# Optimization experiments

Hardware: AMD Instinct MI355X
Metric: run time of the kernel (lower is better)

Reference implementation:

```python
import jax, jax.numpy as jnp
import numpy as np
from jax import lax

B, V, H, W = 8, 3, 512, 640


def setup_inputs() -> dict:
    key = jax.random.key(0)
    k1, k2, k3 = jax.random.split(key, 3)
    # predicted depths in a realistic positive range
    pred_pts = jax.random.uniform(k1, (B, V, H, W), jnp.float32, 1.0, 10.0)
    # pinhole intrinsics embedded in 4x4 (invertible)
    f = 500.0
    K1 = jnp.array([[f, 0.0, (W - 1) / 2.0, 0.0],
                    [0.0, f, (H - 1) / 2.0, 0.0],
                    [0.0, 0.0, 1.0, 0.0],
                    [0.0, 0.0, 0.0, 1.0]], jnp.float32)
    K = jnp.broadcast_to(K1, (B, 4, 4))
    # near-identity rotations (QR of I + small noise) + small translations
    A = jnp.eye(3, dtype=jnp.float32) + 0.05 * jax.random.normal(k2, (B, V, 3, 3), jnp.float32)
    Q, R = jnp.linalg.qr(A)
    Q = Q * jnp.sign(jnp.diagonal(R, axis1=-2, axis2=-1))[..., None, :]
    t = 0.1 * jax.random.normal(k3, (B, V, 3), jnp.float32)
    RT = (jnp.zeros((B, V, 4, 4), jnp.float32)
          .at[..., :3, :3].set(Q)
          .at[..., :3, 3].set(t)
          .at[..., 3, 3].set(1.0))
    return {"pred_pts": pred_pts, "K": K, "input_RTs": RT}


def _bilinear_sample(img_flat, gx, gy, h, w):
    """grid_sample(mode=bilinear, align_corners=False, padding=zeros).
    img_flat: (B, H*W); gx, gy: (B, N) in [-1, 1] grid coords."""
    ix = ((gx + 1.0) * w - 1.0) * 0.5
    iy = ((gy + 1.0) * h - 1.0) * 0.5
    x0f = jnp.floor(ix)
    y0f = jnp.floor(iy)
    wx1 = ix - x0f
    wy1 = iy - y0f
    x0 = x0f.astype(jnp.int32)
    y0 = y0f.astype(jnp.int32)

    def corner(xi, yi):
        valid = (xi >= 0) & (xi < w) & (yi >= 0) & (yi < h)
        idx = jnp.clip(yi, 0, h - 1) * w + jnp.clip(xi, 0, w - 1)
        val = jnp.take_along_axis(img_flat, idx, axis=1)
        return jnp.where(valid, val, 0.0)

    return ((1.0 - wy1) * (1.0 - wx1) * corner(x0, y0)
            + (1.0 - wy1) * wx1 * corner(x0 + 1, y0)
            + wy1 * (1.0 - wx1) * corner(x0, y0 + 1)
            + wy1 * wx1 * corner(x0 + 1, y0 + 1))


def reference(pred_pts, K, input_RTs):
    b, v, h, w = pred_pts.shape
    dt = pred_pts.dtype
    yy, xx = jnp.meshgrid(jnp.arange(h, dtype=dt), jnp.arange(w, dtype=dt), indexing='ij')
    x = xx.reshape(-1)  # (HW,)
    y = yy.reshape(-1)
    Kinv = jnp.linalg.inv(K)            # (B,4,4)
    RTinv = jnp.linalg.inv(input_RTs)   # (B,V,4,4)

    total = jnp.zeros((), dt)
    for i in range(v):
        for j in range(v):
            d = pred_pts[:, i].reshape(b, -1)          # (B, HW)
            ones = jnp.ones_like(d)
            # homogeneous coords (x*d, y*d, d, 1): (B, 4, HW)
            xyz = jnp.stack([x[None] * d, y[None] * d, d, ones], axis=1)
            # composed projection: K @ RT_j @ inv(RT_i) @ inv(K)  (same math as chained bmms)
            P = jnp.einsum('bij,bjk,bkl,blm->bim', K, input_RTs[:, j], RTinv[:, i], Kinv)
            proj = jnp.einsum('bij,bjn->bin', P, xyz)  # (B, 4, HW)
            proj = proj / proj[:, 3:4]
            projected_depth = proj[:, 2]               # (B, HW)
            gx = proj[:, 0] / ((w - 1) / 2.0) - 1.0
            gy = proj[:, 1] / ((h - 1) / 2.0) - 1.0
            mask = ((gx >= -1.0) & (gx <= 1.0) & (gy >= -1.0) & (gy <= 1.0)).astype(dt)
            warped = _bilinear_sample(pred_pts[:, j].reshape(b, -1), gx, gy, h, w)
            num = jnp.sum(jnp.abs(warped - projected_depth) * mask)
            den = jnp.maximum(jnp.sum(mask), 1.0)
            total = total + num / den
    return total
```

## Files before the change

### kernel.cpp

```cpp
#include <hip/hip_runtime.h>

#define Bn 8
#define Vn 3
#define Hn 512
#define Wn 640
#define Nn (Hn * Wn)
#define PX 16
#define TPB 256
#define XBLKS (Nn / (TPB * PX))
#define GRIDN (XBLKS * Vn * Bn)

struct __attribute__((aligned(4))) fpair { float a, b; };

__device__ __forceinline__ float rfl(float x) {
    return __int_as_float(__builtin_amdgcn_readfirstlane(__float_as_int(x)));
}

__device__ __forceinline__ void computeQ(const float* __restrict__ K,
                                         const float* __restrict__ RT,
                                         int b, int i, float Q[Vn][12]) {
    const float* Kb = K + (size_t)b * 16;
    const float f  = Kb[0], cx = Kb[2], cy = Kb[6];
    const float rf = 1.0f / f;
    const float* Ti = RT + (size_t)(b * Vn + i) * 16;
    const float A00=Ti[0], A01=Ti[1], A02=Ti[2],  A03=Ti[3];
    const float A10=Ti[4], A11=Ti[5], A12=Ti[6],  A13=Ti[7];
    const float A20=Ti[8], A21=Ti[9], A22=Ti[10], A23=Ti[11];
    const float I00=A00, I01=A10, I02=A20, I03=-(A00*A03 + A10*A13 + A20*A23);
    const float I10=A01, I11=A11, I12=A21, I13=-(A01*A03 + A11*A13 + A21*A23);
    const float I20=A02, I21=A12, I22=A22, I23=-(A02*A03 + A12*A13 + A22*A23);
    #pragma unroll
    for (int j = 0; j < Vn; ++j) {
        const float* Tj = RT + (size_t)(b * Vn + j) * 16;
        const float B00=Tj[0], B01=Tj[1], B02=Tj[2],  B03=Tj[3];
        const float B10=Tj[4], B11=Tj[5], B12=Tj[6],  B13=Tj[7];
        const float B20=Tj[8], B21=Tj[9], B22=Tj[10], B23=Tj[11];
        const float M00=B00*I00+B01*I10+B02*I20, M01=B00*I01+B01*I11+B02*I21,
                    M02=B00*I02+B01*I12+B02*I22, M03=B00*I03+B01*I13+B02*I23+B03;
        const float M10=B10*I00+B11*I10+B12*I20, M11=B10*I01+B11*I11+B12*I21,
                    M12=B10*I02+B11*I12+B12*I22, M13=B10*I03+B11*I13+B12*I23+B13;
        const float M20=B20*I00+B21*I10+B22*I20, M21=B20*I01+B21*I11+B22*I21,
                    M22=B20*I02+B21*I12+B22*I22, M23=B20*I03+B21*I13+B22*I23+B23;
        const float G00=f*M00+cx*M20, G01=f*M01+cx*M21, G02=f*M02+cx*M22, G03=f*M03+cx*M23;
        const float G10=f*M10+cy*M20, G11=f*M11+cy*M21, G12=f*M12+cy*M22, G13=f*M13+cy*M23;
        const float G20=M20,          G21=M21,          G22=M22,          G23=M23;
        Q[j][0]  = rfl(G00*rf);  Q[j][1]  = rfl(G01*rf);
        Q[j][2]  = rfl(G02 - (cx*rf)*G00 - (cy*rf)*G01);  Q[j][3]  = rfl(G03);
        Q[j][4]  = rfl(G10*rf);  Q[j][5]  = rfl(G11*rf);
        Q[j][6]  = rfl(G12 - (cx*rf)*G10 - (cy*rf)*G11);  Q[j][7]  = rfl(G13);
        Q[j][8]  = rfl(G20*rf);  Q[j][9]  = rfl(G21*rf);
        Q[j][10] = rfl(G22 - (cx*rf)*G20 - (cy*rf)*G21);  Q[j][11] = rfl(G23);
    }
}

__global__ __launch_bounds__(TPB, 8) void loss_main_kernel(const float* __restrict__ pred,
                                                           const float* __restrict__ K,
                                                           const float* __restrict__ RT,
                                                           float* __restrict__ part) {
    const int id   = blockIdx.x;
    const int b    = id & 7;
    const int r    = id >> 3;
    const int i    = r % Vn;
    const int xblk = r / Vn;

    float Q[Vn][12];
    computeQ(K, RT, b, i, Q);

    const int tid  = threadIdx.x;
    const int h    = (xblk >= 40) ? 1 : 0;
    const int c0   = xblk - 40 * h;
    const int yrow = 2 * tid + h;
    int c = c0 + tid;
    c -= (c / 40) * 40;
    const int xcol = c << 4;
    const int base = yrow * Wn + xcol;
    const float fy = (float)yrow;

    const float* dptr = pred + (size_t)(b * Vn + i) * Nn + base;
    float dv[PX];
    {
        const float4 a0 = *reinterpret_cast<const float4*>(dptr);
        const float4 a1 = *reinterpret_cast<const float4*>(dptr + 4);
        const float4 a2 = *reinterpret_cast<const float4*>(dptr + 8);
        const float4 a3 = *reinterpret_cast<const float4*>(dptr + 12);
        dv[0]=a0.x; dv[1]=a0.y; dv[2]=a0.z; dv[3]=a0.w;
        dv[4]=a1.x; dv[5]=a1.y; dv[6]=a1.z; dv[7]=a1.w;
        dv[8]=a2.x; dv[9]=a2.y; dv[10]=a2.z; dv[11]=a2.w;
        dv[12]=a3.x; dv[13]=a3.y; dv[14]=a3.z; dv[15]=a3.w;
    }

    const float cW = (float)Wn / (float)(Wn - 1);
    const float cH = (float)Hn / (float)(Hn - 1);

    float num[Vn] = {0.0f, 0.0f, 0.0f};
    float den[Vn] = {0.0f, 0.0f, 0.0f};

    #pragma unroll
    for (int j = 0; j < Vn; ++j) {
        const float* __restrict__ img = pred + (size_t)(b * Vn + j) * Nn;
        const float rx = fmaf(Q[j][1], fy, Q[j][2]);
        const float ry = fmaf(Q[j][5], fy, Q[j][6]);
        const float rz = fmaf(Q[j][9], fy, Q[j][10]);

        #pragma unroll
        for (int k = 0; k < PX; ++k) {
            const float d  = dv[k];
            const float fx = (float)(xcol + k);

            const float X = fmaf(d, fmaf(Q[j][0], fx, rx), Q[j][3]);
            const float Y = fmaf(d, fmaf(Q[j][4], fx, ry), Q[j][7]);
            const float Z = fmaf(d, fmaf(Q[j][8], fx, rz), Q[j][11]);

            const bool inb = (X >= 0.0f) & (X <= (float)(Wn - 1)) &
                             (Y >= 0.0f) & (Y <= (float)(Hn - 1));
            if (inb) {
                const float ix = fmaf(X, cW, -0.5f);
                const float iy = fmaf(Y, cH, -0.5f);
                const float x0f = floorf(ix);
                const float y0f = floorf(iy);
                const float wx1 = ix - x0f;
                const float wy1 = iy - y0f;
                const float wx0 = 1.0f - wx1;
                const float wy0 = 1.0f - wy1;
                const int x0 = (int)x0f;
                const int y0 = (int)y0f;
                const bool border = (x0 < 0) | (x0 > Wn - 2) | (y0 < 0) | (y0 > Hn - 2);
                float warped;
                if (__ballot(border) == 0ull) {
                    const int ad = y0 * Wn + x0;
                    const fpair q0 = *reinterpret_cast<const fpair*>(img + ad);
                    const fpair q1 = *reinterpret_cast<const fpair*>(img + ad + Wn);
                    warped = wy0 * fmaf(wx0, q0.a, wx1 * q0.b)
                           + wy1 * fmaf(wx0, q1.a, wx1 * q1.b);
                } else {
                    const int x1 = x0 + 1;
                    const int y1 = y0 + 1;
                    const int cy0 = max(y0, 0);
                    const int cy1 = min(y1, Hn - 1);
                    const int cx  = min(max(x0, 0), Wn - 2);
                    const bool xlo = (x0 >= 0);
                    const bool xhi = (x0 <= Wn - 2);
                    const fpair q0 = *reinterpret_cast<const fpair*>(img + (cy0 * Wn + cx));
                    const fpair q1 = *reinterpret_cast<const fpair*>(img + (cy1 * Wn + cx));
                    const float c00 = xhi ? q0.a : q0.b;
                    const float c10 = xlo ? q0.b : q0.a;
                    const float c01 = xhi ? q1.a : q1.b;
                    const float c11 = xlo ? q1.b : q1.a;
                    const float wx0v = xlo ? wx0 : 0.0f;
                    const float wx1v = (x1 < Wn) ? wx1 : 0.0f;
                    const float wy0v = (y0 >= 0) ? wy0 : 0.0f;
                    const float wy1v = (y1 < Hn) ? wy1 : 0.0f;
                    warped = wy0v * fmaf(wx0v, c00, wx1v * c10)
                           + wy1v * fmaf(wx0v, c01, wx1v * c11);
                }
                num[j] += fabsf(warped - Z);
                den[j] += 1.0f;
            }
        }
    }

    #pragma unroll
    for (int off = 32; off > 0; off >>= 1) {
        #pragma unroll
        for (int j = 0; j < Vn; ++j) {
            num[j] += __shfl_down(num[j], off, 64);
            den[j] += __shfl_down(den[j], off, 64);
        }
    }
    __shared__ float s_red[4][2 * Vn];
    const int lane = threadIdx.x & 63;
    const int wid  = threadIdx.x >> 6;
    if (lane == 0) {
        #pragma unroll
        for (int j = 0; j < Vn; ++j) {
            s_red[wid][2 * j + 0] = num[j];
            s_red[wid][2 * j + 1] = den[j];
        }
    }
    __syncthreads();
    if (threadIdx.x < 2 * Vn) {
        const int slot = threadIdx.x;
        const float v = s_red[0][slot] + s_red[1][slot] + s_red[2][slot] + s_red[3][slot];
        part[(size_t)id * 8 + slot] = v;
    }
}

__global__ __launch_bounds__(TPB) void finalize_kernel(const float* __restrict__ part,
                                                       float* __restrict__ out) {
    float acc[2 * Vn * Vn];
    #pragma unroll
    for (int s = 0; s < 2 * Vn * Vn; ++s) acc[s] = 0.0f;

    for (int m = threadIdx.x; m < GRIDN; m += TPB) {
        const int i = (m >> 3) % Vn;
        const float* pp = part + (size_t)m * 8;
        #pragma unroll
        for (int j = 0; j < Vn; ++j) {
            acc[(i * Vn + j) * 2 + 0] += pp[2 * j + 0];
            acc[(i * Vn + j) * 2 + 1] += pp[2 * j + 1];
        }
    }
    #pragma unroll
    for (int off = 32; off > 0; off >>= 1) {
        #pragma unroll
        for (int s = 0; s < 2 * Vn * Vn; ++s)
            acc[s] += __shfl_down(acc[s], off, 64);
    }
    __shared__ float s_fin[4][2 * Vn * Vn];
    const int lane = threadIdx.x & 63;
    const int wid  = threadIdx.x >> 6;
    if (lane == 0) {
        #pragma unroll
        for (int s = 0; s < 2 * Vn * Vn; ++s) s_fin[wid][s] = acc[s];
    }
    __syncthreads();
    if (threadIdx.x == 0) {
        float t = 0.0f;
        #pragma unroll
        for (int pr = 0; pr < Vn * Vn; ++pr) {
            const float nn = s_fin[0][pr*2+0] + s_fin[1][pr*2+0] + s_fin[2][pr*2+0] + s_fin[3][pr*2+0];
            const float dd = s_fin[0][pr*2+1] + s_fin[1][pr*2+1] + s_fin[2][pr*2+1] + s_fin[3][pr*2+1];
            t += nn / fmaxf(dd, 1.0f);
        }
        out[0] = t;
    }
}

extern "C" void kernel_launch(void* const* d_in, const int* in_sizes, int n_in,
                              void* d_out, int out_size, void* d_ws, size_t ws_size,
                              hipStream_t stream) {
    const float* pred = (const float*)d_in[0];
    const float* K    = (const float*)d_in[1];
    const float* RT   = (const float*)d_in[2];
    float* out = (float*)d_out;

    float* part = (float*)d_ws;

    loss_main_kernel<<<GRIDN, TPB, 0, stream>>>(pred, K, RT, part);
    finalize_kernel<<<1, TPB, 0, stream>>>(part, out);
}
```

Baseline: 113.2 us.

## Interleave adjacent rows in a prepass so bilinear gathers use one float4 load

Adds a prepass kernel that writes each depth plane into a workspace layout interleaving row y and row y+1 per pixel. The interior bilinear path can then fetch all four corners with a single 16-byte aligned load instead of two 8-byte loads from different rows. The cost is an extra kernel that reads the whole input and writes a buffer twice its size (about 63 MB), plus a larger footprint for the gathers in the main kernel.

```diff
diff --git a/kernel.cpp b/kernel.cpp
--- a/kernel.cpp
+++ b/kernel.cpp
@@ -10,10 +10,37 @@
 #define XBLKS (Nn / (TPB * PX))
 #define GRIDN (XBLKS * Vn * Bn)
 
+#define JSTRIDE (2 * Nn)
+#define JOFF_PART (64 * 1024 * 1024 / 4)
+
+#define PRE_TPB 256
+#define PRE_UNITS (Bn * Vn * Nn / 8)
+#define PRE_GRID (PRE_UNITS / PRE_TPB)
+
 struct __attribute__((aligned(4))) fpair { float a, b; };
 
 __device__ __forceinline__ float rfl(float x) {
     return __int_as_float(__builtin_amdgcn_readfirstlane(__float_as_int(x)));
+}
+
+__global__ __launch_bounds__(PRE_TPB) void prepass_kernel(const float* __restrict__ pred,
+                                                          float* __restrict__ J) {
+    const int p     = blockIdx.x * PRE_TPB + threadIdx.x;
+    const int plane = p / (Nn / 8);
+    const int rem   = p - plane * (Nn / 8);
+    const int y     = rem / (Wn / 8);
+    const int x8    = (rem - y * (Wn / 8)) * 8;
+    const float* src = pred + (size_t)plane * Nn;
+    const int yn = (y < Hn - 1) ? y + 1 : y;
+    const float4 r0a = *reinterpret_cast<const float4*>(src + y  * Wn + x8);
+    const float4 r0b = *reinterpret_cast<const float4*>(src + y  * Wn + x8 + 4);
+    const float4 r1a = *reinterpret_cast<const float4*>(src + yn * Wn + x8);
+    const float4 r1b = *reinterpret_cast<const float4*>(src + yn * Wn + x8 + 4);
+    float* dst = J + (size_t)plane * JSTRIDE + 2 * (y * Wn + x8);
+    reinterpret_cast<float4*>(dst)[0] = make_float4(r0a.x, r1a.x, r0a.y, r1a.y);
+    reinterpret_cast<float4*>(dst)[1] = make_float4(r0a.z, r1a.z, r0a.w, r1a.w);
+    reinterpret_cast<float4*>(dst)[2] = make_float4(r0b.x, r1b.x, r0b.y, r1b.y);
+    reinterpret_cast<float4*>(dst)[3] = make_float4(r0b.z, r1b.z, r0b.w, r1b.w);
 }
 
 __device__ __forceinline__ void computeQ(const float* __restrict__ K,
@@ -54,6 +81,7 @@
 }
 
 __global__ __launch_bounds__(TPB, 8) void loss_main_kernel(const float* __restrict__ pred,
+                                                           const float* __restrict__ J,
                                                            const float* __restrict__ K,
                                                            const float* __restrict__ RT,
                                                            float* __restrict__ part) {
@@ -98,6 +126,7 @@
     #pragma unroll
     for (int j = 0; j < Vn; ++j) {
         const float* __restrict__ img = pred + (size_t)(b * Vn + j) * Nn;
+        const float* __restrict__ Jb  = J    + (size_t)(b * Vn + j) * JSTRIDE;
         const float rx = fmaf(Q[j][1], fy, Q[j][2]);
         const float ry = fmaf(Q[j][5], fy, Q[j][6]);
         const float rz = fmaf(Q[j][9], fy, Q[j][10]);
@@ -127,11 +156,10 @@
                 const bool border = (x0 < 0) | (x0 > Wn - 2) | (y0 < 0) | (y0 > Hn - 2);
                 float warped;
                 if (__ballot(border) == 0ull) {
-                    const int ad = y0 * Wn + x0;
-                    const fpair q0 = *reinterpret_cast<const fpair*>(img + ad);
-                    const fpair q1 = *reinterpret_cast<const fpair*>(img + ad + Wn);
-                    warped = wy0 * fmaf(wx0, q0.a, wx1 * q0.b)
-                           + wy1 * fmaf(wx0, q1.a, wx1 * q1.b);
+                    const float* qp = Jb + ((y0 * Wn + x0) << 1);
+                    const float4 q = *reinterpret_cast<const float4*>(qp);
+                    warped = wy0 * fmaf(wx0, q.x, wx1 * q.z)
+                           + wy1 * fmaf(wx0, q.y, wx1 * q.w);
                 } else {
                     const int x1 = x0 + 1;
                     const int y1 = y0 + 1;
@@ -234,8 +262,10 @@
     const float* RT   = (const float*)d_in[2];
     float* out = (float*)d_out;
 
-    float* part = (float*)d_ws;
-
-    loss_main_kernel<<<GRIDN, TPB, 0, stream>>>(pred, K, RT, part);
+    float* J    = (float*)d_ws;
+    float* part = (float*)d_ws + JOFF_PART;
+
+    prepass_kernel<<<PRE_GRID, PRE_TPB, 0, stream>>>(pred, J);
+    loss_main_kernel<<<GRIDN, TPB, 0, stream>>>(pred, J, K, RT, part);
     finalize_kernel<<<1, TPB, 0, stream>>>(part, out);
 }
```

Result: slower. 136.0 us (+20.2%).

## Pack vertical pixel pairs into fp16 half2 planes for single-load bilinear gathers

Applied to the files above, without the earlier changes.

A new prepass kernel converts each depth plane into an interleaved fp16 layout where each element holds a pixel and the pixel below it. The interior bilinear path then fetches all four corners with one 8-byte load instead of two separate row loads. This removes one gather per sample and halves the gather footprint, at the cost of an extra full pass over the input and reduced precision in the sampled depths.

```diff
diff --git a/kernel.cpp b/kernel.cpp
--- a/kernel.cpp
+++ b/kernel.cpp
@@ -1,4 +1,5 @@
 #include <hip/hip_runtime.h>
+#include <hip/hip_fp16.h>
 
 #define Bn 8
 #define Vn 3
@@ -10,10 +11,35 @@
 #define XBLKS (Nn / (TPB * PX))
 #define GRIDN (XBLKS * Vn * Bn)
 
+#define JOFF_PART (64 * 1024 * 1024 / 4)
+#define PRE_TPB 256
+#define PRE_UNITS (Bn * Vn * Nn / 4)
+#define PRE_GRID (PRE_UNITS / PRE_TPB)
+
 struct __attribute__((aligned(4))) fpair { float a, b; };
+struct __attribute__((aligned(4))) h2q { __half2 r0, r1; };
 
 __device__ __forceinline__ float rfl(float x) {
     return __int_as_float(__builtin_amdgcn_readfirstlane(__float_as_int(x)));
+}
+
+__global__ __launch_bounds__(PRE_TPB) void prepass_kernel(const float* __restrict__ pred,
+                                                          __half2* __restrict__ J16) {
+    const int t     = blockIdx.x * PRE_TPB + threadIdx.x;
+    const int plane = t / (Nn / 4);
+    const int rem   = t - plane * (Nn / 4);
+    const int y     = rem / (Wn / 4);
+    const int x4    = (rem - y * (Wn / 4)) * 4;
+    const float* src = pred + (size_t)plane * Nn;
+    const int yn = (y < Hn - 1) ? y + 1 : y;
+    const float4 r0 = *reinterpret_cast<const float4*>(src + y  * Wn + x4);
+    const float4 r1 = *reinterpret_cast<const float4*>(src + yn * Wn + x4);
+    struct __attribute__((aligned(16))) h2x4 { __half2 a, b, c, d; } o;
+    o.a = __floats2half2_rn(r0.x, r1.x);
+    o.b = __floats2half2_rn(r0.y, r1.y);
+    o.c = __floats2half2_rn(r0.z, r1.z);
+    o.d = __floats2half2_rn(r0.w, r1.w);
+    *reinterpret_cast<h2x4*>(J16 + (size_t)plane * Nn + y * Wn + x4) = o;
 }
 
 __device__ __forceinline__ void computeQ(const float* __restrict__ K,
@@ -54,6 +80,7 @@
 }
 
 __global__ __launch_bounds__(TPB, 8) void loss_main_kernel(const float* __restrict__ pred,
+                                                           const __half2* __restrict__ J16,
                                                            const float* __restrict__ K,
                                                            const float* __restrict__ RT,
                                                            float* __restrict__ part) {
@@ -97,7 +124,8 @@
 
     #pragma unroll
     for (int j = 0; j < Vn; ++j) {
-        const float* __restrict__ img = pred + (size_t)(b * Vn + j) * Nn;
+        const float* __restrict__ img  = pred + (size_t)(b * Vn + j) * Nn;
+        const __half2* __restrict__ Jb = J16  + (size_t)(b * Vn + j) * Nn;
         const float rx = fmaf(Q[j][1], fy, Q[j][2]);
         const float ry = fmaf(Q[j][5], fy, Q[j][6]);
         const float rz = fmaf(Q[j][9], fy, Q[j][10]);
@@ -127,11 +155,13 @@
                 const bool border = (x0 < 0) | (x0 > Wn - 2) | (y0 < 0) | (y0 > Hn - 2);
                 float warped;
                 if (__ballot(border) == 0ull) {
-                    const int ad = y0 * Wn + x0;
-                    const fpair q0 = *reinterpret_cast<const fpair*>(img + ad);
-                    const fpair q1 = *reinterpret_cast<const fpair*>(img + ad + Wn);
-                    warped = wy0 * fmaf(wx0, q0.a, wx1 * q0.b)
-                           + wy1 * fmaf(wx0, q1.a, wx1 * q1.b);
+                    const h2q q = *reinterpret_cast<const h2q*>(Jb + (y0 * Wn + x0));
+                    const float c00 = __low2float(q.r0);
+                    const float c01 = __high2float(q.r0);
+                    const float c10 = __low2float(q.r1);
+                    const float c11 = __high2float(q.r1);
+                    warped = wy0 * fmaf(wx0, c00, wx1 * c10)
+                           + wy1 * fmaf(wx0, c01, wx1 * c11);
                 } else {
                     const int x1 = x0 + 1;
                     const int y1 = y0 + 1;
@@ -234,8 +264,10 @@
     const float* RT   = (const float*)d_in[2];
     float* out = (float*)d_out;
 
-    float* part = (float*)d_ws;
-
-    loss_main_kernel<<<GRIDN, TPB, 0, stream>>>(pred, K, RT, part);
+    __half2* J16 = (__half2*)d_ws;
+    float*   part = (float*)d_ws + JOFF_PART;
+
+    prepass_kernel<<<PRE_GRID, PRE_TPB, 0, stream>>>(pred, J16);
+    loss_main_kernel<<<GRIDN, TPB, 0, stream>>>(pred, J16, K, RT, part);
     finalize_kernel<<<1, TPB, 0, stream>>>(part, out);
 }
```

Measured after the change: 125.4 us. +10.8%, slower.
